# Performance work log

Measured on AMD Instinct MI355X. Metric: run time of the kernel, lower is better.

The kernel has to match this reference:

```python
import jax, jax.numpy as jnp
import numpy as np

B, S, HID = 1, 2048, 4096
NH, NKV, D = 32, 8, 128
SCALE = D ** -0.5


def _rope_tables(seq_len, head_dim, base=10000.0):
    inv_freq = 1.0 / (base ** (jnp.arange(0, head_dim, 2, dtype=jnp.float32) / head_dim))
    freqs = jnp.arange(seq_len, dtype=jnp.float32)[:, None] * inv_freq[None, :]  # [S, D/2]
    emb = jnp.concatenate([freqs, freqs], axis=-1)  # [S, D]
    return jnp.cos(emb), jnp.sin(emb)


def _rotate_half(x):
    half = x.shape[-1] // 2
    return jnp.concatenate([-x[..., half:], x[..., :half]], axis=-1)


def setup_inputs() -> dict:
    key = jax.random.key(0)
    ks = jax.random.split(key, 5)
    hidden = jax.random.normal(ks[0], (B, S, HID), dtype=jnp.float32)
    cos, sin = _rope_tables(S, D)
    # additive causal mask: 0 on/below diagonal, large negative above
    neg = jnp.full((S, S), -1e9, dtype=jnp.float32)
    causal_mask = jnp.triu(neg, k=1)[None, None]  # [1,1,S,S]
    std_in = HID ** -0.5
    Wq = jax.random.normal(ks[1], (HID, NH * D), dtype=jnp.float32) * std_in
    Wk = jax.random.normal(ks[2], (HID, NKV * D), dtype=jnp.float32) * std_in
    Wv = jax.random.normal(ks[3], (HID, NKV * D), dtype=jnp.float32) * std_in
    Wo = jax.random.normal(ks[4], (NH * D, HID), dtype=jnp.float32) * ((NH * D) ** -0.5)
    return {"hidden": hidden, "cos": cos, "sin": sin, "causal_mask": causal_mask,
            "Wq": Wq, "Wk": Wk, "Wv": Wv, "Wo": Wo}


def reference(hidden, cos, sin, causal_mask, Wq, Wk, Wv, Wo):
    b, s, _ = hidden.shape
    q = (hidden @ Wq).reshape(b, s, NH, D).transpose(0, 2, 1, 3)    # [B,H,S,D]
    k = (hidden @ Wk).reshape(b, s, NKV, D).transpose(0, 2, 1, 3)   # [B,Hkv,S,D]
    v = (hidden @ Wv).reshape(b, s, NKV, D).transpose(0, 2, 1, 3)
    c = cos[None, None]  # [1,1,S,D]
    sn = sin[None, None]
    q = q * c + _rotate_half(q) * sn
    k = k * c + _rotate_half(k) * sn
    group = NH // NKV
    if group > 1:
        k = jnp.repeat(k, group, axis=1)  # [B,H,S,D]
        v = jnp.repeat(v, group, axis=1)
    scores = jnp.einsum('bhsd,bhtd->bhst', q, k) * SCALE + causal_mask
    attn = jax.nn.softmax(scores.astype(jnp.float32), axis=-1).astype(v.dtype)
    ctx = jnp.einsum('bhst,bhtd->bhsd', attn, v)
    ctx = ctx.transpose(0, 2, 1, 3).reshape(b, s, NH * D)
    return ctx @ Wo
```

## Files before the change

### kernel.cpp

```cpp
#include <hip/hip_runtime.h>
#include <hip/hip_bf16.h>
#include <cstdint>
#include <cstddef>

typedef __attribute__((ext_vector_type(8))) short bf16x8;
typedef __attribute__((ext_vector_type(4))) float f32x4;
typedef __attribute__((ext_vector_type(4))) unsigned int u32x4;

__device__ __forceinline__ unsigned short f2bf(float f) {
  __hip_bfloat16 h = __float2bfloat16(f);
  return *reinterpret_cast<unsigned short*>(&h);
}
__device__ __forceinline__ float bf2f(unsigned short u) {
  __hip_bfloat16 h = *reinterpret_cast<__hip_bfloat16*>(&u);
  return __bfloat162float(h);
}

typedef const __attribute__((address_space(1))) void gas_void;
typedef __attribute__((address_space(3))) void las_void;
__device__ __forceinline__ void gload_lds16(const void* g, void* l) {
  __builtin_amdgcn_global_load_lds((gas_void*)g, (las_void*)l, 16, 0, 0);
}

template <int N>
__device__ __forceinline__ void waitcnt_vm() {
  asm volatile("s_waitcnt vmcnt(%0)" :: "i"(N) : "memory");
}
#define LGKM0 { asm volatile("s_waitcnt lgkmcnt(0)" ::: "memory"); \
                __builtin_amdgcn_sched_barrier(0); }

#define S_LEN 2048
#define HID 4096
#define NH 32
#define NKV 8
#define HD 128
#define NQKV 6144
static const float ATT_SCALE = 0.08838834764831845f;


__global__ void prep_kernel(const float* __restrict__ hidden, short* __restrict__ hid_bf,
                            const float* __restrict__ Wq, const float* __restrict__ Wk,
                            const float* __restrict__ Wv, const float* __restrict__ Wo,
                            short* __restrict__ Wcat, short* __restrict__ WoT) {
  __shared__ float tile[64][33];
  const int bid = blockIdx.x;
  const int t = threadIdx.x;
  if (bid >= 20480) {
    int i = ((bid - 20480) * 256 + t) * 8;
    f32x4 a = *(const f32x4*)(hidden + i);
    f32x4 b = *(const f32x4*)(hidden + i + 4);
    unsigned short o[8];
#pragma unroll
    for (int k = 0; k < 4; ++k) { o[k] = f2bf(a[k]); o[4 + k] = f2bf(b[k]); }
    *(u32x4*)(hid_bf + i) = *(const u32x4*)o;
    return;
  }
  const float* src; short* dst; int N, loc;
  if (bid < 8192)       { src = Wq; dst = Wcat;                      N = 4096; loc = bid; }
  else if (bid < 10240) { src = Wk; dst = Wcat + (size_t)4096 * HID; N = 1024; loc = bid - 8192; }
  else if (bid < 12288) { src = Wv; dst = Wcat + (size_t)5120 * HID; N = 1024; loc = bid - 10240; }
  else                  { src = Wo; dst = WoT;                       N = 4096; loc = bid - 12288; }
  const int kb = (loc & 63) * 64, nb = (loc >> 6) * 32;
  {
    int kr = t >> 3, c4 = (t & 7) * 4;
#pragma unroll
    for (int i = 0; i < 2; ++i) {
      int k = kr + i * 32;
      f32x4 v = *(const f32x4*)(src + (size_t)(kb + k) * N + nb + c4);
      tile[k][c4] = v[0]; tile[k][c4 + 1] = v[1];
      tile[k][c4 + 2] = v[2]; tile[k][c4 + 3] = v[3];
    }
  }
  __syncthreads();
  int n = t >> 3, k0 = (t & 7) * 8;
  unsigned short o[8];
#pragma unroll
  for (int i = 0; i < 8; ++i) o[i] = f2bf(tile[k0 + i][n]);
  *(u32x4*)(dst + (size_t)(nb + n) * HID + kb + k0) = *(const u32x4*)o;
}


#define READ_A(MHL) { \
    const short* As_ = lds + (kt & 1) * BUF; \
    _Pragma("unroll") for (int m = 0; m < MHALF; ++m) \
    _Pragma("unroll") for (int kk = 0; kk < 2; ++kk) { \
      int row = (MHL) * (BM / 2) + wr * MSTEP + m * 16 + r; \
      int c = kk * 4 + g; \
      af[m][kk] = *(const bf16x8*)(As_ + row * 64 + ((c ^ (row & 7)) * 8)); \
    } }
#define READ_B(NHL) { \
    const short* Bs_ = lds + (kt & 1) * BUF + BM * 64; \
    _Pragma("unroll") for (int n = 0; n < NHALF; ++n) \
    _Pragma("unroll") for (int kk = 0; kk < 2; ++kk) { \
      int row = (NHL) * (BN / 2) + wc * NSTEP + n * 16 + r; \
      int c = kk * 4 + g; \
      bf[n][kk] = *(const bf16x8*)(Bs_ + row * 64 + ((c ^ (row & 7)) * 8)); \
    } }
#define MFMA_QUAD(MHL, NHL) { \
    __builtin_amdgcn_s_setprio(1); \
    _Pragma("unroll") for (int m = 0; m < MHALF; ++m) \
    _Pragma("unroll") for (int n = 0; n < NHALF; ++n) \
    _Pragma("unroll") for (int kk = 0; kk < 2; ++kk) \
      acc[(MHL)*MHALF + m][(NHL)*NHALF + n] = __builtin_amdgcn_mfma_f32_16x16x32_bf16( \
          af[m][kk], bf[n][kk], acc[(MHL)*MHALF + m][(NHL)*NHALF + n], 0, 0, 0); \
    __builtin_amdgcn_s_setprio(0); }

template <int MODE, int BM, int BN, int WM, int WN>
__global__ __launch_bounds__(WM * WN * 64, 2) void gemm8p_kernel(
    const short* __restrict__ A, const short* __restrict__ Bt,
    int M, int N, int K,
    float* __restrict__ Cf, short* __restrict__ qb_,
    short* __restrict__ kb_, short* __restrict__ vb_) {
  constexpr int NT = WM * WN * 64;
  constexpr int M_FR = BM / (WM * 16);
  constexpr int N_FR = BN / (WN * 16);
  constexpr int MHALF = M_FR / 2;
  constexpr int NHALF = N_FR / 2;
  constexpr int MSTEP = BM / (2 * WM);
  constexpr int NSTEP = BN / (2 * WN);
  constexpr int LA = (BM / 2) * 8 / NT;
  constexpr int LB = (BN / 2) * 8 / NT;
  constexpr int BUF = (BM + BN) * 64;

  __shared__ short lds[2 * BUF];

  const int tid = threadIdx.x, wid = tid >> 6, lane = tid & 63;
  const int wr = wid / WN, wc = wid % WN;
  const int r = lane & 15, g = lane >> 4;
  const int brow = blockIdx.y * BM, bcol = blockIdx.x * BN;
  const int T = K >> 6;

  f32x4 acc[M_FR][N_FR] = {};
  bf16x8 af[MHALF][2], bf[NHALF][2];

  auto stage_rgn = [&](int kt, int rgn) {
    short* buf = lds + (kt & 1) * BUF;
    if (rgn == 0 || rgn == 3) {
      const int mh = (rgn == 3);
      short* dst = buf + mh * (BM / 2) * 64;
      const short* src = A + (size_t)(brow + mh * (BM / 2)) * K + kt * 64;
#pragma unroll
      for (int i = 0; i < LA; ++i) {
        int slot = i * NT + tid;
        int row = slot >> 3, c2 = slot & 7;
        gload_lds16(src + (size_t)row * K + ((c2 ^ (row & 7)) * 8), dst + slot * 8);
      }
    } else {
      const int nh = (rgn == 2);
      short* dst = buf + BM * 64 + nh * (BN / 2) * 64;
      const short* src = Bt + (size_t)(bcol + nh * (BN / 2)) * K + kt * 64;
#pragma unroll
      for (int i = 0; i < LB; ++i) {
        int slot = i * NT + tid;
        int row = slot >> 3, c2 = slot & 7;
        gload_lds16(src + (size_t)row * K + ((c2 ^ (row & 7)) * 8), dst + slot * 8);
      }
    }
  };

  stage_rgn(0, 0); stage_rgn(0, 1); stage_rgn(0, 2); stage_rgn(0, 3);

  for (int kt = 0; kt < T; ++kt) {
    const bool nl = (kt + 1 < T);
    waitcnt_vm<0>();
    __builtin_amdgcn_s_barrier();
    __builtin_amdgcn_sched_barrier(0);
    READ_A(0); READ_B(0);
    if (nl) { stage_rgn(kt + 1, 0); stage_rgn(kt + 1, 1);
              stage_rgn(kt + 1, 2); stage_rgn(kt + 1, 3); }
    LGKM0;
    MFMA_QUAD(0, 0);
    READ_B(1);
    LGKM0;
    MFMA_QUAD(0, 1);
    READ_A(1);
    LGKM0;
    MFMA_QUAD(1, 1);
    READ_B(0);
    LGKM0;
    MFMA_QUAD(1, 0);
  }

  if (MODE == 0) {
#pragma unroll
    for (int fm = 0; fm < M_FR; ++fm)
#pragma unroll
      for (int fn = 0; fn < N_FR; ++fn)
#pragma unroll
        for (int j = 0; j < 4; ++j) {
          int row = brow + (fm / MHALF) * (BM / 2) + wr * MSTEP + (fm % MHALF) * 16 + g * 4 + j;
          int col = bcol + (fn / NHALF) * (BN / 2) + wc * NSTEP + (fn % NHALF) * 16 + r;
          Cf[(size_t)row * N + col] = acc[fm][fn][j];
        }
  } else {
#pragma unroll
    for (int fn = 0; fn < N_FR; ++fn) {
      const int cb = bcol + (fn / NHALF) * (BN / 2) + wc * NSTEP + (fn % NHALF) * 16;
      if (cb < 4096) {
        unsigned short* dst = (unsigned short*)qb_ + (size_t)(cb >> 7) * S_LEN * HD;
        const int d0 = cb & 127;
#pragma unroll
        for (int fm = 0; fm < M_FR; ++fm)
#pragma unroll
          for (int j = 0; j < 4; ++j) {
            int row = brow + (fm / MHALF) * (BM / 2) + wr * MSTEP + (fm % MHALF) * 16 + g * 4 + j;
            dst[(size_t)row * HD + d0 + r] = f2bf(acc[fm][fn][j]);
          }
      } else if (cb < 5120) {
        char* base = (char*)kb_ + ((size_t)((cb - 4096) >> 7) << 19);
        const int d = cb & 127;
#pragma unroll
        for (int fm = 0; fm < M_FR; ++fm)
#pragma unroll
          for (int j = 0; j < 4; ++j) {
            int row = brow + (fm / MHALF) * (BM / 2) + wr * MSTEP + (fm % MHALF) * 16 + g * 4 + j;
            int dd = d + r;
            int krow = row & 63;
            size_t off = ((size_t)(row >> 6) << 14) +
                         ((((krow << 8) + ((dd >> 3) << 4)) ^ ((krow & 7) << 4)) + ((dd & 7) << 1));
            *(unsigned short*)(base + off) = f2bf(acc[fm][fn][j]);
          }
      } else {
        char* base = (char*)vb_ + ((size_t)((cb - 5120) >> 7) << 19);
        const int d = cb & 127;
#pragma unroll
        for (int fm = 0; fm < M_FR; ++fm)
#pragma unroll
          for (int j = 0; j < 4; ++j) {
            int row = brow + (fm / MHALF) * (BM / 2) + wr * MSTEP + (fm % MHALF) * 16 + g * 4 + j;
            int dd = d + r;
            int sl = row & 63;
            size_t off = ((size_t)(row >> 6) << 14) +
                         ((((dd << 7) + ((sl >> 3) << 4)) ^ ((dd & 7) << 4)) + ((sl & 7) << 1));
            *(unsigned short*)(base + off) = f2bf(acc[fm][fn][j]);
          }
      }
    }
  }
}

__global__ void rope_kernel(short* __restrict__ qbuf, short* __restrict__ kbuf,
                            const float* __restrict__ cosT, const float* __restrict__ sinT) {
  int idx = blockIdx.x * 256 + threadIdx.x;
  const int total = (NH + NKV) * S_LEN * 64;
  if (idx >= total) return;
  int d = idx & 63;
  int rowi = idx >> 6;
  int s;
  unsigned short *p1, *p2;
  if (rowi < NH * S_LEN) {
    unsigned short* base = (unsigned short*)qbuf + (size_t)rowi * HD;
    s = rowi & (S_LEN - 1);
    p1 = base + d; p2 = base + d + 64;
  } else {
    int kr = rowi - NH * S_LEN;
    int kvh = kr >> 11; s = kr & (S_LEN - 1);
    char* base = (char*)kbuf + ((size_t)kvh << 19) + ((size_t)(s >> 6) << 14);
    int krow = s & 63, swz = (krow & 7) << 4;
    int dd = d + 64;
    p1 = (unsigned short*)(base + ((((krow << 8) + ((d >> 3) << 4)) ^ swz) + ((d & 7) << 1)));
    p2 = (unsigned short*)(base + ((((krow << 8) + ((dd >> 3) << 4)) ^ swz) + ((dd & 7) << 1)));
  }
  float x1 = bf2f(*p1);
  float x2 = bf2f(*p2);
  float c1 = cosT[s * HD + d], s1 = sinT[s * HD + d];
  *p1 = f2bf(x1 * c1 - x2 * s1);
  *p2 = f2bf(x2 * c1 + x1 * s1);
}

__global__ __launch_bounds__(512, 2) void attn_kernel(const short* __restrict__ qb_,
                                                      const short* __restrict__ kb_,
                                                      const short* __restrict__ vb_,
                                                      short* __restrict__ ctx) {
  const int bid = blockIdx.x;
  const int kvh = bid & 7;
  const int idx = bid >> 3;
  const int h = kvh * 4 + (idx & 3);
  const int slot = idx >> 2;
  const int tid = threadIdx.x, wid = tid >> 6, lane = tid & 63;
  const int r = lane & 15, g = lane >> 4;

  __shared__ short Ks[2][64 * 128];
  __shared__ short Vts[2][128 * 64];
  __shared__ short Ps[8][16 * 64];

  const int qb2s[2] = { slot, 15 - slot };
  const int nt0 = 2 * qb2s[0] + 2;
  const int T = 34;

  const char* kvbase_k = (const char*)kb_ + ((size_t)kvh << 19);
  const char* kvbase_v = (const char*)vb_ + ((size_t)kvh << 19);

  auto stage = [&](int tg, int b) {
    int kvt = (tg < nt0) ? tg : (tg - nt0);
    const char* kt = kvbase_k + ((size_t)kvt << 14);
    const char* vt = kvbase_v + ((size_t)kvt << 14);
#pragma unroll
    for (int i = 0; i < 2; ++i) {
      int ch = i * 8 + wid;
      gload_lds16(kt + ch * 1024 + lane * 16, (char*)&Ks[b][0] + ch * 1024);
      gload_lds16(vt + ch * 1024 + lane * 16, (char*)&Vts[b][0] + ch * 1024);
    }
  };

  stage(0, 0);
  int cur = 0, tglob = 0;

  for (int sec = 0; sec < 2; ++sec) {
    const int qb2 = qb2s[sec];
    const int nt = 2 * qb2 + 2;
    const int rowbase = qb2 * 128 + wid * 16;

    const unsigned short* qptr =
        (const unsigned short*)qb_ + ((size_t)h * S_LEN + rowbase) * HD;
    bf16x8 qf[4];
#pragma unroll
    for (int s4 = 0; s4 < 4; ++s4)
      qf[s4] = *(const bf16x8*)(qptr + (size_t)r * HD + s4 * 32 + g * 8);

    f32x4 oacc[8] = {};
    float m_run[4], l_run[4];
#pragma unroll
    for (int j = 0; j < 4; ++j) { m_run[j] = -1e30f; l_run[j] = 0.f; }

    for (int kvt = 0; kvt < nt; ++kvt, ++tglob) {
      __syncthreads();
      if (tglob + 1 < T) stage(tglob + 1, cur ^ 1);

      const char* Kc = (const char*)&Ks[cur][0];
      const char* Vc = (const char*)&Vts[cur][0];

      f32x4 sv[4] = {};
      __builtin_amdgcn_s_setprio(1);
#pragma unroll
      for (int n = 0; n < 4; ++n) {
        int krow = n * 16 + r;
        int swz = (krow & 7) << 4;
#pragma unroll
        for (int s4 = 0; s4 < 4; ++s4) {
          bf16x8 kf = *(const bf16x8*)(Kc + ((krow * 256 + s4 * 64 + g * 16) ^ swz));
          sv[n] = __builtin_amdgcn_mfma_f32_16x16x32_bf16(qf[s4], kf, sv[n], 0, 0, 0);
        }
      }
      __builtin_amdgcn_s_setprio(0);

      if (kvt * 64 + 63 > rowbase) {
#pragma unroll
        for (int n = 0; n < 4; ++n)
#pragma unroll
          for (int j = 0; j < 4; ++j) {
            int colg = kvt * 64 + n * 16 + r;
            int rowg = rowbase + g * 4 + j;
            sv[n][j] = (colg <= rowg) ? sv[n][j] * ATT_SCALE : -1e30f;
          }
      } else {
#pragma unroll
        for (int n = 0; n < 4; ++n)
#pragma unroll
          for (int j = 0; j < 4; ++j) sv[n][j] *= ATT_SCALE;
      }

      float pmax[4];
#pragma unroll
      for (int j = 0; j < 4; ++j)
        pmax[j] = fmaxf(fmaxf(sv[0][j], sv[1][j]), fmaxf(sv[2][j], sv[3][j]));
#pragma unroll
      for (int msk = 1; msk <= 8; msk <<= 1)
#pragma unroll
        for (int j = 0; j < 4; ++j) pmax[j] = fmaxf(pmax[j], __shfl_xor(pmax[j], msk));

      float sf[4], rsum[4];
#pragma unroll
      for (int j = 0; j < 4; ++j) {
        float mn = fmaxf(m_run[j], pmax[j]);
        sf[j] = __expf(m_run[j] - mn);
        m_run[j] = mn;
        rsum[j] = 0.f;
      }
#pragma unroll
      for (int n = 0; n < 4; ++n)
#pragma unroll
        for (int j = 0; j < 4; ++j) {
          float p = __expf(sv[n][j] - m_run[j]);
          sv[n][j] = p;
          rsum[j] += p;
        }
#pragma unroll
      for (int msk = 1; msk <= 8; msk <<= 1)
#pragma unroll
        for (int j = 0; j < 4; ++j) rsum[j] += __shfl_xor(rsum[j], msk);
#pragma unroll
      for (int j = 0; j < 4; ++j) l_run[j] = l_run[j] * sf[j] + rsum[j];
#pragma unroll
      for (int t = 0; t < 8; ++t)
#pragma unroll
        for (int j = 0; j < 4; ++j) oacc[t][j] *= sf[j];

#pragma unroll
      for (int n = 0; n < 4; ++n)
#pragma unroll
        for (int j = 0; j < 4; ++j) {
          int prow = g * 4 + j, pcol = n * 16 + r;
          int poff = (prow * 128 + pcol * 2) ^ ((prow & 7) << 4);
          *(unsigned short*)((char*)&Ps[wid][0] + poff) = f2bf(sv[n][j]);
        }

      __builtin_amdgcn_s_setprio(1);
#pragma unroll
      for (int s4 = 0; s4 < 2; ++s4) {
        bf16x8 pf = *(const bf16x8*)((const char*)&Ps[wid][0] +
                                     ((r * 128 + s4 * 64 + g * 16) ^ ((r & 7) << 4)));
#pragma unroll
        for (int t = 0; t < 8; ++t) {
          int vrow = t * 16 + r;
          bf16x8 vf = *(const bf16x8*)(Vc + ((vrow * 128 + s4 * 64 + g * 16) ^ ((vrow & 7) << 4)));
          oacc[t] = __builtin_amdgcn_mfma_f32_16x16x32_bf16(pf, vf, oacc[t], 0, 0, 0);
        }
      }
      __builtin_amdgcn_s_setprio(0);
      cur ^= 1;
    }

    float inv[4];
#pragma unroll
    for (int j = 0; j < 4; ++j) inv[j] = 1.0f / l_run[j];
#pragma unroll
    for (int t = 0; t < 8; ++t)
#pragma unroll
      for (int j = 0; j < 4; ++j) {
        int rowg = rowbase + g * 4 + j;
        int colg = h * HD + t * 16 + r;
        ((unsigned short*)ctx)[(size_t)rowg * HID + colg] = f2bf(oacc[t][j] * inv[j]);
      }
  }
}

extern "C" void kernel_launch(void* const* d_in, const int* in_sizes, int n_in,
                              void* d_out, int out_size, void* d_ws, size_t ws_size,
                              hipStream_t stream) {
  const float* hidden = (const float*)d_in[0];
  const float* cosT   = (const float*)d_in[1];
  const float* sinT   = (const float*)d_in[2];
  const float* Wq = (const float*)d_in[4];
  const float* Wk = (const float*)d_in[5];
  const float* Wv = (const float*)d_in[6];
  const float* Wo = (const float*)d_in[7];
  float* out = (float*)d_out;

  char* ws = (char*)d_ws;
  short* hid_bf = (short*)(ws);
  short* Wcat   = (short*)(ws + 16777216);
  short* WoT    = (short*)(ws + 67108864);
  short* qbuf   = (short*)(ws + 100663296);
  short* kbuf   = (short*)(ws + 117440512);
  short* vbuf   = (short*)(ws + 121634816);
  short* ctx    = (short*)(ws + 125829120);

  prep_kernel<<<24576, 256, 0, stream>>>(hidden, hid_bf, Wq, Wk, Wv, Wo, Wcat, WoT);

  gemm8p_kernel<1, 128, 384, 2, 4><<<dim3(16, 16), 512, 0, stream>>>(
      hid_bf, Wcat, S_LEN, NQKV, HID, nullptr, qbuf, kbuf, vbuf);

  rope_kernel<<<20480, 256, 0, stream>>>(qbuf, kbuf, cosT, sinT);

  attn_kernel<<<256, 512, 0, stream>>>(qbuf, kbuf, vbuf, ctx);

  gemm8p_kernel<0, 128, 256, 2, 4><<<dim3(16, 16), 512, 0, stream>>>(
      ctx, WoT, S_LEN, HID, HID, out, nullptr, nullptr, nullptr);
}
```

Measured before the change: 320.0 us.

## Switch GEMM kernels from 16x16x32 to 32x32x16 bf16 MFMA tiles

```diff
diff --git a/kernel.cpp b/kernel.cpp
--- a/kernel.cpp
+++ b/kernel.cpp
@@ -5,6 +5,7 @@
 
 typedef __attribute__((ext_vector_type(8))) short bf16x8;
 typedef __attribute__((ext_vector_type(4))) float f32x4;
+typedef __attribute__((ext_vector_type(16))) float f32x16;
 typedef __attribute__((ext_vector_type(4))) unsigned int u32x4;
 
 __device__ __forceinline__ unsigned short f2bf(float f) {
@@ -26,8 +27,6 @@
 __device__ __forceinline__ void waitcnt_vm() {
   asm volatile("s_waitcnt vmcnt(%0)" :: "i"(N) : "memory");
 }
-#define LGKM0 { asm volatile("s_waitcnt lgkmcnt(0)" ::: "memory"); \
-                __builtin_amdgcn_sched_barrier(0); }
 
 #define S_LEN 2048
 #define HID 4096
@@ -80,44 +79,15 @@
 }
 
 
-#define READ_A(MHL) { \
-    const short* As_ = lds + (kt & 1) * BUF; \
-    _Pragma("unroll") for (int m = 0; m < MHALF; ++m) \
-    _Pragma("unroll") for (int kk = 0; kk < 2; ++kk) { \
-      int row = (MHL) * (BM / 2) + wr * MSTEP + m * 16 + r; \
-      int c = kk * 4 + g; \
-      af[m][kk] = *(const bf16x8*)(As_ + row * 64 + ((c ^ (row & 7)) * 8)); \
-    } }
-#define READ_B(NHL) { \
-    const short* Bs_ = lds + (kt & 1) * BUF + BM * 64; \
-    _Pragma("unroll") for (int n = 0; n < NHALF; ++n) \
-    _Pragma("unroll") for (int kk = 0; kk < 2; ++kk) { \
-      int row = (NHL) * (BN / 2) + wc * NSTEP + n * 16 + r; \
-      int c = kk * 4 + g; \
-      bf[n][kk] = *(const bf16x8*)(Bs_ + row * 64 + ((c ^ (row & 7)) * 8)); \
-    } }
-#define MFMA_QUAD(MHL, NHL) { \
-    __builtin_amdgcn_s_setprio(1); \
-    _Pragma("unroll") for (int m = 0; m < MHALF; ++m) \
-    _Pragma("unroll") for (int n = 0; n < NHALF; ++n) \
-    _Pragma("unroll") for (int kk = 0; kk < 2; ++kk) \
-      acc[(MHL)*MHALF + m][(NHL)*NHALF + n] = __builtin_amdgcn_mfma_f32_16x16x32_bf16( \
-          af[m][kk], bf[n][kk], acc[(MHL)*MHALF + m][(NHL)*NHALF + n], 0, 0, 0); \
-    __builtin_amdgcn_s_setprio(0); }
-
 template <int MODE, int BM, int BN, int WM, int WN>
-__global__ __launch_bounds__(WM * WN * 64, 2) void gemm8p_kernel(
+__global__ __launch_bounds__(WM * WN * 64, 2) void gemm32_kernel(
     const short* __restrict__ A, const short* __restrict__ Bt,
     int M, int N, int K,
     float* __restrict__ Cf, short* __restrict__ qb_,
     short* __restrict__ kb_, short* __restrict__ vb_) {
   constexpr int NT = WM * WN * 64;
-  constexpr int M_FR = BM / (WM * 16);
-  constexpr int N_FR = BN / (WN * 16);
-  constexpr int MHALF = M_FR / 2;
-  constexpr int NHALF = N_FR / 2;
-  constexpr int MSTEP = BM / (2 * WM);
-  constexpr int NSTEP = BN / (2 * WN);
+  constexpr int MT = BM / (WM * 32);
+  constexpr int NTL = BN / (WN * 32);
   constexpr int LA = (BM / 2) * 8 / NT;
   constexpr int LB = (BN / 2) * 8 / NT;
   constexpr int BUF = (BM + BN) * 64;
@@ -126,12 +96,11 @@
 
   const int tid = threadIdx.x, wid = tid >> 6, lane = tid & 63;
   const int wr = wid / WN, wc = wid % WN;
-  const int r = lane & 15, g = lane >> 4;
+  const int l31 = lane & 31, lh = lane >> 5;
   const int brow = blockIdx.y * BM, bcol = blockIdx.x * BN;
   const int T = K >> 6;
 
-  f32x4 acc[M_FR][N_FR] = {};
-  bf16x8 af[MHALF][2], bf[NHALF][2];
+  f32x16 acc[MT][NTL] = {};
 
   auto stage_rgn = [&](int kt, int rgn) {
     short* buf = lds + (kt & 1) * BUF;
@@ -165,74 +134,84 @@
     waitcnt_vm<0>();
     __builtin_amdgcn_s_barrier();
     __builtin_amdgcn_sched_barrier(0);
-    READ_A(0); READ_B(0);
     if (nl) { stage_rgn(kt + 1, 0); stage_rgn(kt + 1, 1);
               stage_rgn(kt + 1, 2); stage_rgn(kt + 1, 3); }
-    LGKM0;
-    MFMA_QUAD(0, 0);
-    READ_B(1);
-    LGKM0;
-    MFMA_QUAD(0, 1);
-    READ_A(1);
-    LGKM0;
-    MFMA_QUAD(1, 1);
-    READ_B(0);
-    LGKM0;
-    MFMA_QUAD(1, 0);
+
+    const short* As_ = lds + (kt & 1) * BUF;
+    const short* Bs_ = As_ + BM * 64;
+#pragma unroll
+    for (int st = 0; st < 4; ++st) {
+      bf16x8 af[MT], bf[NTL];
+      const int c = st * 2 + lh;
+#pragma unroll
+      for (int mt = 0; mt < MT; ++mt) {
+        int row = wr * (BM / WM) + mt * 32 + l31;
+        af[mt] = *(const bf16x8*)(As_ + row * 64 + ((c ^ (row & 7)) * 8));
+      }
+#pragma unroll
+      for (int nt = 0; nt < NTL; ++nt) {
+        int row = wc * (BN / WN) + nt * 32 + l31;
+        bf[nt] = *(const bf16x8*)(Bs_ + row * 64 + ((c ^ (row & 7)) * 8));
+      }
+      __builtin_amdgcn_s_setprio(1);
+#pragma unroll
+      for (int mt = 0; mt < MT; ++mt)
+#pragma unroll
+        for (int nt = 0; nt < NTL; ++nt)
+          acc[mt][nt] = __builtin_amdgcn_mfma_f32_32x32x16_bf16(
+              af[mt], bf[nt], acc[mt][nt], 0, 0, 0);
+      __builtin_amdgcn_s_setprio(0);
+    }
   }
 
   if (MODE == 0) {
 #pragma unroll
-    for (int fm = 0; fm < M_FR; ++fm)
-#pragma unroll
-      for (int fn = 0; fn < N_FR; ++fn)
-#pragma unroll
-        for (int j = 0; j < 4; ++j) {
-          int row = brow + (fm / MHALF) * (BM / 2) + wr * MSTEP + (fm % MHALF) * 16 + g * 4 + j;
-          int col = bcol + (fn / NHALF) * (BN / 2) + wc * NSTEP + (fn % NHALF) * 16 + r;
-          Cf[(size_t)row * N + col] = acc[fm][fn][j];
+    for (int mt = 0; mt < MT; ++mt)
+#pragma unroll
+      for (int nt = 0; nt < NTL; ++nt)
+#pragma unroll
+        for (int reg = 0; reg < 16; ++reg) {
+          int row = brow + wr * (BM / WM) + mt * 32 + (reg & 3) + 8 * (reg >> 2) + 4 * lh;
+          int col = bcol + wc * (BN / WN) + nt * 32 + l31;
+          Cf[(size_t)row * N + col] = acc[mt][nt][reg];
         }
   } else {
 #pragma unroll
-    for (int fn = 0; fn < N_FR; ++fn) {
-      const int cb = bcol + (fn / NHALF) * (BN / 2) + wc * NSTEP + (fn % NHALF) * 16;
+    for (int nt = 0; nt < NTL; ++nt) {
+      const int cb = bcol + wc * (BN / WN) + nt * 32;
+      const int d = (cb & 127) + l31;
       if (cb < 4096) {
         unsigned short* dst = (unsigned short*)qb_ + (size_t)(cb >> 7) * S_LEN * HD;
-        const int d0 = cb & 127;
-#pragma unroll
-        for (int fm = 0; fm < M_FR; ++fm)
-#pragma unroll
-          for (int j = 0; j < 4; ++j) {
-            int row = brow + (fm / MHALF) * (BM / 2) + wr * MSTEP + (fm % MHALF) * 16 + g * 4 + j;
-            dst[(size_t)row * HD + d0 + r] = f2bf(acc[fm][fn][j]);
+#pragma unroll
+        for (int mt = 0; mt < MT; ++mt)
+#pragma unroll
+          for (int reg = 0; reg < 16; ++reg) {
+            int row = brow + wr * (BM / WM) + mt * 32 + (reg & 3) + 8 * (reg >> 2) + 4 * lh;
+            dst[(size_t)row * HD + d] = f2bf(acc[mt][nt][reg]);
           }
       } else if (cb < 5120) {
         char* base = (char*)kb_ + ((size_t)((cb - 4096) >> 7) << 19);
-        const int d = cb & 127;
-#pragma unroll
-        for (int fm = 0; fm < M_FR; ++fm)
-#pragma unroll
-          for (int j = 0; j < 4; ++j) {
-            int row = brow + (fm / MHALF) * (BM / 2) + wr * MSTEP + (fm % MHALF) * 16 + g * 4 + j;
-            int dd = d + r;
+#pragma unroll
+        for (int mt = 0; mt < MT; ++mt)
+#pragma unroll
+          for (int reg = 0; reg < 16; ++reg) {
+            int row = brow + wr * (BM / WM) + mt * 32 + (reg & 3) + 8 * (reg >> 2) + 4 * lh;
             int krow = row & 63;
             size_t off = ((size_t)(row >> 6) << 14) +
-                         ((((krow << 8) + ((dd >> 3) << 4)) ^ ((krow & 7) << 4)) + ((dd & 7) << 1));
-            *(unsigned short*)(base + off) = f2bf(acc[fm][fn][j]);
+                         ((((krow << 8) + ((d >> 3) << 4)) ^ ((krow & 7) << 4)) + ((d & 7) << 1));
+            *(unsigned short*)(base + off) = f2bf(acc[mt][nt][reg]);
           }
       } else {
         char* base = (char*)vb_ + ((size_t)((cb - 5120) >> 7) << 19);
-        const int d = cb & 127;
-#pragma unroll
-        for (int fm = 0; fm < M_FR; ++fm)
-#pragma unroll
-          for (int j = 0; j < 4; ++j) {
-            int row = brow + (fm / MHALF) * (BM / 2) + wr * MSTEP + (fm % MHALF) * 16 + g * 4 + j;
-            int dd = d + r;
+#pragma unroll
+        for (int mt = 0; mt < MT; ++mt)
+#pragma unroll
+          for (int reg = 0; reg < 16; ++reg) {
+            int row = brow + wr * (BM / WM) + mt * 32 + (reg & 3) + 8 * (reg >> 2) + 4 * lh;
             int sl = row & 63;
             size_t off = ((size_t)(row >> 6) << 14) +
-                         ((((dd << 7) + ((sl >> 3) << 4)) ^ ((dd & 7) << 4)) + ((sl & 7) << 1));
-            *(unsigned short*)(base + off) = f2bf(acc[fm][fn][j]);
+                         ((((d << 7) + ((sl >> 3) << 4)) ^ ((d & 7) << 4)) + ((sl & 7) << 1));
+            *(unsigned short*)(base + off) = f2bf(acc[mt][nt][reg]);
           }
       }
     }
@@ -458,13 +437,13 @@
 
   prep_kernel<<<24576, 256, 0, stream>>>(hidden, hid_bf, Wq, Wk, Wv, Wo, Wcat, WoT);
 
-  gemm8p_kernel<1, 128, 384, 2, 4><<<dim3(16, 16), 512, 0, stream>>>(
+  gemm32_kernel<1, 128, 384, 2, 4><<<dim3(16, 16), 512, 0, stream>>>(
       hid_bf, Wcat, S_LEN, NQKV, HID, nullptr, qbuf, kbuf, vbuf);
 
   rope_kernel<<<20480, 256, 0, stream>>>(qbuf, kbuf, cosT, sinT);
 
   attn_kernel<<<256, 512, 0, stream>>>(qbuf, kbuf, vbuf, ctx);
 
-  gemm8p_kernel<0, 128, 256, 2, 4><<<dim3(16, 16), 512, 0, stream>>>(
+  gemm32_kernel<0, 128, 256, 2, 4><<<dim3(16, 16), 512, 0, stream>>>(
       ctx, WoT, S_LEN, HID, HID, out, nullptr, nullptr, nullptr);
 }
```

Result: slower. 338.8 us (+5.9%).

## Move Wo transpose-convert from prep kernel into attention kernel tail blocks

Applied to the files above, without the earlier changes.

```diff
diff --git a/kernel.cpp b/kernel.cpp
--- a/kernel.cpp
+++ b/kernel.cpp
@@ -26,8 +26,6 @@
 __device__ __forceinline__ void waitcnt_vm() {
   asm volatile("s_waitcnt vmcnt(%0)" :: "i"(N) : "memory");
 }
-#define LGKM0 { asm volatile("s_waitcnt lgkmcnt(0)" ::: "memory"); \
-                __builtin_amdgcn_sched_barrier(0); }
 
 #define S_LEN 2048
 #define HID 4096
@@ -40,13 +38,13 @@
 
 __global__ void prep_kernel(const float* __restrict__ hidden, short* __restrict__ hid_bf,
                             const float* __restrict__ Wq, const float* __restrict__ Wk,
-                            const float* __restrict__ Wv, const float* __restrict__ Wo,
-                            short* __restrict__ Wcat, short* __restrict__ WoT) {
+                            const float* __restrict__ Wv,
+                            short* __restrict__ Wcat) {
   __shared__ float tile[64][33];
   const int bid = blockIdx.x;
   const int t = threadIdx.x;
-  if (bid >= 20480) {
-    int i = ((bid - 20480) * 256 + t) * 8;
+  if (bid >= 12288) {
+    int i = ((bid - 12288) * 256 + t) * 8;
     f32x4 a = *(const f32x4*)(hidden + i);
     f32x4 b = *(const f32x4*)(hidden + i + 4);
     unsigned short o[8];
@@ -58,8 +56,7 @@
   const float* src; short* dst; int N, loc;
   if (bid < 8192)       { src = Wq; dst = Wcat;                      N = 4096; loc = bid; }
   else if (bid < 10240) { src = Wk; dst = Wcat + (size_t)4096 * HID; N = 1024; loc = bid - 8192; }
-  else if (bid < 12288) { src = Wv; dst = Wcat + (size_t)5120 * HID; N = 1024; loc = bid - 10240; }
-  else                  { src = Wo; dst = WoT;                       N = 4096; loc = bid - 12288; }
+  else                  { src = Wv; dst = Wcat + (size_t)5120 * HID; N = 1024; loc = bid - 10240; }
   const int kb = (loc & 63) * 64, nb = (loc >> 6) * 32;
   {
     int kr = t >> 3, c4 = (t & 7) * 4;
@@ -168,16 +165,20 @@
     READ_A(0); READ_B(0);
     if (nl) { stage_rgn(kt + 1, 0); stage_rgn(kt + 1, 1);
               stage_rgn(kt + 1, 2); stage_rgn(kt + 1, 3); }
-    LGKM0;
+    asm volatile("s_waitcnt lgkmcnt(0)" ::: "memory");
+    __builtin_amdgcn_sched_barrier(0);
     MFMA_QUAD(0, 0);
     READ_B(1);
-    LGKM0;
+    asm volatile("s_waitcnt lgkmcnt(0)" ::: "memory");
+    __builtin_amdgcn_sched_barrier(0);
     MFMA_QUAD(0, 1);
     READ_A(1);
-    LGKM0;
+    asm volatile("s_waitcnt lgkmcnt(0)" ::: "memory");
+    __builtin_amdgcn_sched_barrier(0);
     MFMA_QUAD(1, 1);
     READ_B(0);
-    LGKM0;
+    asm volatile("s_waitcnt lgkmcnt(0)" ::: "memory");
+    __builtin_amdgcn_sched_barrier(0);
     MFMA_QUAD(1, 0);
   }
 
@@ -271,18 +272,47 @@
 __global__ __launch_bounds__(512, 2) void attn_kernel(const short* __restrict__ qb_,
                                                       const short* __restrict__ kb_,
                                                       const short* __restrict__ vb_,
-                                                      short* __restrict__ ctx) {
+                                                      short* __restrict__ ctx,
+                                                      const float* __restrict__ Wo,
+                                                      short* __restrict__ WoT) {
   const int bid = blockIdx.x;
+  const int tid = threadIdx.x;
+
+  __shared__ short Ks[2][64 * 128];
+  __shared__ short Vts[2][128 * 64];
+  __shared__ short Ps[8][16 * 64];
+
+  if (bid >= 256) {
+    float* tf = (float*)&Ks[0][0];
+    const int sub = tid >> 8, tt = tid & 255;
+    float* tile = tf + sub * (64 * 34);
+    const int loc = (bid - 256) * 2 + sub;
+    const int kb = (loc & 63) * 64, nb = (loc >> 6) * 32;
+    {
+      int kr = tt >> 3, c4 = (tt & 7) * 4;
+#pragma unroll
+      for (int i = 0; i < 2; ++i) {
+        int k = kr + i * 32;
+        f32x4 v = *(const f32x4*)(Wo + (size_t)(kb + k) * HID + nb + c4);
+        tile[k * 34 + c4] = v[0]; tile[k * 34 + c4 + 1] = v[1];
+        tile[k * 34 + c4 + 2] = v[2]; tile[k * 34 + c4 + 3] = v[3];
+      }
+    }
+    __syncthreads();
+    int n = tt >> 3, k0 = (tt & 7) * 8;
+    unsigned short o[8];
+#pragma unroll
+    for (int i = 0; i < 8; ++i) o[i] = f2bf(tile[(k0 + i) * 34 + n]);
+    *(u32x4*)(WoT + (size_t)(nb + n) * HID + kb + k0) = *(const u32x4*)o;
+    return;
+  }
+
   const int kvh = bid & 7;
   const int idx = bid >> 3;
   const int h = kvh * 4 + (idx & 3);
   const int slot = idx >> 2;
-  const int tid = threadIdx.x, wid = tid >> 6, lane = tid & 63;
+  const int wid = tid >> 6, lane = tid & 63;
   const int r = lane & 15, g = lane >> 4;
-
-  __shared__ short Ks[2][64 * 128];
-  __shared__ short Vts[2][128 * 64];
-  __shared__ short Ps[8][16 * 64];
 
   const int qb2s[2] = { slot, 15 - slot };
   const int nt0 = 2 * qb2s[0] + 2;
@@ -456,14 +486,14 @@
   short* vbuf   = (short*)(ws + 121634816);
   short* ctx    = (short*)(ws + 125829120);
 
-  prep_kernel<<<24576, 256, 0, stream>>>(hidden, hid_bf, Wq, Wk, Wv, Wo, Wcat, WoT);
+  prep_kernel<<<16384, 256, 0, stream>>>(hidden, hid_bf, Wq, Wk, Wv, Wcat);
 
   gemm8p_kernel<1, 128, 384, 2, 4><<<dim3(16, 16), 512, 0, stream>>>(
       hid_bf, Wcat, S_LEN, NQKV, HID, nullptr, qbuf, kbuf, vbuf);
 
   rope_kernel<<<20480, 256, 0, stream>>>(qbuf, kbuf, cosT, sinT);
 
-  attn_kernel<<<256, 512, 0, stream>>>(qbuf, kbuf, vbuf, ctx);
+  attn_kernel<<<4352, 512, 0, stream>>>(qbuf, kbuf, vbuf, ctx, Wo, WoT);
 
   gemm8p_kernel<0, 128, 256, 2, 4><<<dim3(16, 16), 512, 0, stream>>>(
       ctx, WoT, S_LEN, HID, HID, out, nullptr, nullptr, nullptr);
```

Result: no change. 321.6 us (+0.5%).

## Fuse Q RoPE into attention kernel and shrink attention blocks to 4 waves

Applied to the files above, without the earlier changes.

```diff
diff --git a/kernel.cpp b/kernel.cpp
--- a/kernel.cpp
+++ b/kernel.cpp
@@ -78,7 +78,6 @@
   for (int i = 0; i < 8; ++i) o[i] = f2bf(tile[k0 + i][n]);
   *(u32x4*)(dst + (size_t)(nb + n) * HID + kb + k0) = *(const u32x4*)o;
 }
-
 
 #define READ_A(MHL) { \
     const short* As_ = lds + (kt & 1) * BUF; \
@@ -239,28 +238,19 @@
   }
 }
 
-__global__ void rope_kernel(short* __restrict__ qbuf, short* __restrict__ kbuf,
+__global__ void rope_kernel(short* __restrict__ kbuf,
                             const float* __restrict__ cosT, const float* __restrict__ sinT) {
   int idx = blockIdx.x * 256 + threadIdx.x;
-  const int total = (NH + NKV) * S_LEN * 64;
+  const int total = NKV * S_LEN * 64;
   if (idx >= total) return;
   int d = idx & 63;
-  int rowi = idx >> 6;
-  int s;
-  unsigned short *p1, *p2;
-  if (rowi < NH * S_LEN) {
-    unsigned short* base = (unsigned short*)qbuf + (size_t)rowi * HD;
-    s = rowi & (S_LEN - 1);
-    p1 = base + d; p2 = base + d + 64;
-  } else {
-    int kr = rowi - NH * S_LEN;
-    int kvh = kr >> 11; s = kr & (S_LEN - 1);
-    char* base = (char*)kbuf + ((size_t)kvh << 19) + ((size_t)(s >> 6) << 14);
-    int krow = s & 63, swz = (krow & 7) << 4;
-    int dd = d + 64;
-    p1 = (unsigned short*)(base + ((((krow << 8) + ((d >> 3) << 4)) ^ swz) + ((d & 7) << 1)));
-    p2 = (unsigned short*)(base + ((((krow << 8) + ((dd >> 3) << 4)) ^ swz) + ((dd & 7) << 1)));
-  }
+  int kr = idx >> 6;
+  int kvh = kr >> 11, s = kr & (S_LEN - 1);
+  char* base = (char*)kbuf + ((size_t)kvh << 19) + ((size_t)(s >> 6) << 14);
+  int krow = s & 63, swz = (krow & 7) << 4;
+  int dd = d + 64;
+  unsigned short* p1 = (unsigned short*)(base + ((((krow << 8) + ((d >> 3) << 4)) ^ swz) + ((d & 7) << 1)));
+  unsigned short* p2 = (unsigned short*)(base + ((((krow << 8) + ((dd >> 3) << 4)) ^ swz) + ((dd & 7) << 1)));
   float x1 = bf2f(*p1);
   float x2 = bf2f(*p2);
   float c1 = cosT[s * HD + d], s1 = sinT[s * HD + d];
@@ -268,10 +258,12 @@
   *p2 = f2bf(x2 * c1 + x1 * s1);
 }
 
-__global__ __launch_bounds__(512, 2) void attn_kernel(const short* __restrict__ qb_,
+__global__ __launch_bounds__(256, 2) void attn_kernel(const short* __restrict__ qb_,
                                                       const short* __restrict__ kb_,
                                                       const short* __restrict__ vb_,
-                                                      short* __restrict__ ctx) {
+                                                      short* __restrict__ ctx,
+                                                      const float* __restrict__ cosT,
+                                                      const float* __restrict__ sinT) {
   const int bid = blockIdx.x;
   const int kvh = bid & 7;
   const int idx = bid >> 3;
@@ -282,10 +274,10 @@
 
   __shared__ short Ks[2][64 * 128];
   __shared__ short Vts[2][128 * 64];
-  __shared__ short Ps[8][16 * 64];
-
-  const int qb2s[2] = { slot, 15 - slot };
-  const int nt0 = 2 * qb2s[0] + 2;
+  __shared__ short Ps[4][16 * 64];
+
+  const int qb2s[2] = { slot, 31 - slot };
+  const int nt0 = qb2s[0] + 1;
   const int T = 34;
 
   const char* kvbase_k = (const char*)kb_ + ((size_t)kvh << 19);
@@ -296,8 +288,8 @@
     const char* kt = kvbase_k + ((size_t)kvt << 14);
     const char* vt = kvbase_v + ((size_t)kvt << 14);
 #pragma unroll
-    for (int i = 0; i < 2; ++i) {
-      int ch = i * 8 + wid;
+    for (int i = 0; i < 4; ++i) {
+      int ch = i * 4 + wid;
       gload_lds16(kt + ch * 1024 + lane * 16, (char*)&Ks[b][0] + ch * 1024);
       gload_lds16(vt + ch * 1024 + lane * 16, (char*)&Vts[b][0] + ch * 1024);
     }
@@ -308,8 +300,8 @@
 
   for (int sec = 0; sec < 2; ++sec) {
     const int qb2 = qb2s[sec];
-    const int nt = 2 * qb2 + 2;
-    const int rowbase = qb2 * 128 + wid * 16;
+    const int nt = qb2 + 1;
+    const int rowbase = qb2 * 64 + wid * 16;
 
     const unsigned short* qptr =
         (const unsigned short*)qb_ + ((size_t)h * S_LEN + rowbase) * HD;
@@ -317,6 +309,28 @@
 #pragma unroll
     for (int s4 = 0; s4 < 4; ++s4)
       qf[s4] = *(const bf16x8*)(qptr + (size_t)r * HD + s4 * 32 + g * 8);
+
+    {
+      const int s = rowbase + r;
+      const float* cp = cosT + (size_t)s * HD + g * 8;
+      const float* sp = sinT + (size_t)s * HD + g * 8;
+#pragma unroll
+      for (int s4 = 0; s4 < 2; ++s4) {
+        f32x4 c0 = *(const f32x4*)(cp + s4 * 32);
+        f32x4 c1 = *(const f32x4*)(cp + s4 * 32 + 4);
+        f32x4 sn0 = *(const f32x4*)(sp + s4 * 32);
+        f32x4 sn1 = *(const f32x4*)(sp + s4 * 32 + 4);
+#pragma unroll
+        for (int j = 0; j < 8; ++j) {
+          float cc = (j < 4) ? c0[j & 3] : c1[j & 3];
+          float ss = (j < 4) ? sn0[j & 3] : sn1[j & 3];
+          float x1 = bf2f((unsigned short)qf[s4][j]);
+          float x2 = bf2f((unsigned short)qf[s4 + 2][j]);
+          qf[s4][j] = (short)f2bf(x1 * cc - x2 * ss);
+          qf[s4 + 2][j] = (short)f2bf(x2 * cc + x1 * ss);
+        }
+      }
+    }
 
     f32x4 oacc[8] = {};
     float m_run[4], l_run[4];
@@ -461,9 +475,9 @@
   gemm8p_kernel<1, 128, 384, 2, 4><<<dim3(16, 16), 512, 0, stream>>>(
       hid_bf, Wcat, S_LEN, NQKV, HID, nullptr, qbuf, kbuf, vbuf);
 
-  rope_kernel<<<20480, 256, 0, stream>>>(qbuf, kbuf, cosT, sinT);
-
-  attn_kernel<<<256, 512, 0, stream>>>(qbuf, kbuf, vbuf, ctx);
+  rope_kernel<<<4096, 256, 0, stream>>>(kbuf, cosT, sinT);
+
+  attn_kernel<<<512, 256, 0, stream>>>(qbuf, kbuf, vbuf, ctx, cosT, sinT);
 
   gemm8p_kernel<0, 128, 256, 2, 4><<<dim3(16, 16), 512, 0, stream>>>(
       ctx, WoT, S_LEN, HID, HID, out, nullptr, nullptr, nullptr);
```

After: 314.4 us. No clear change (-1.7%).
